# Performance work log

Hardware: AMD Instinct MI355X
Metric: run time of the kernel (lower is better)

Reference implementation:

```python
import jax, jax.numpy as jnp
import numpy as np

NUM_BINS = 30
MIN_BW = 0.001
MIN_BH = 0.001
MIN_D = 0.001
LI, UI = 0.0, 1.0   # input bounds
LO, UO = 0.0, 1.0   # output bounds
DERIV_OUT = (UO - LO) / (UI - LI)
EPS = 1e-6


def _cumparams(unnorm, lower, upper, min_size):
    # softmax -> min-size floor -> cumsum -> pad zero -> affine to [lower, upper]
    p = jax.nn.softmax(unnorm, axis=-1)
    p = min_size + (1.0 - min_size * NUM_BINS) * p
    cp = jnp.cumsum(p, axis=-1)
    cp = jnp.pad(cp, [(0, 0), (1, 0)])            # [V, nb+1], starts at 0
    cp = (upper - lower) * cp + lower
    return cp, cp[..., 1:] - cp[..., :-1]         # cum, bin sizes


def _spline_forward(inputs, uw, uh, ud):
    V = uw.shape[0]
    cw, widths = _cumparams(uw, LI, UI, MIN_BW)   # [V, nb+1], [V, nb]
    ch, heights = _cumparams(uh, LO, UO, MIN_BH)

    # boundary derivative constant: softplus(c) = 1 - MIN_D  =>  deriv = 1 at edges
    c = np.log(np.exp(1.0 - MIN_D) - 1.0).astype(np.float32)
    edge = jnp.full((V, 1), c, dtype=uw.dtype)
    derivs = MIN_D + jax.nn.softplus(jnp.concatenate([edge, ud, edge], axis=-1))  # [V, nb+1]

    delta = heights / widths                      # [V, nb]
    cb = cw.at[..., -1].add(EPS)                  # bin-search boundaries

    below = inputs < LI
    above = inputs > UI
    inside = ~(below | above)
    x = jnp.clip(inputs, LI, UI)                  # safe values for masked-out points

    # per-point bin search: [B, V, nb+1] comparison then sum
    bin_idx = jnp.sum(x[..., None] >= cb[None], axis=-1) - 1
    bin_idx = jnp.clip(bin_idx, 0, NUM_BINS - 1)  # [B, V] int

    v = jnp.arange(V)[None, :]
    icw = cw[v, bin_idx]
    ibw = widths[v, bin_idx]
    ich = ch[v, bin_idx]
    idl = delta[v, bin_idx]
    d0 = derivs[v, bin_idx]
    d1 = derivs[v, bin_idx + 1]
    ih = heights[v, bin_idx]

    theta = (x - icw) / ibw
    t1mt = theta * (1.0 - theta)
    den = idl + (d0 + d1 - 2.0 * idl) * t1mt
    out_in = ich + ih * (idl * theta * theta + d0 * t1mt) / den
    numd = (idl * idl) * (d1 * theta * theta + 2.0 * idl * t1mt + d0 * (1.0 - theta) ** 2)
    lad_in = jnp.log(numd) - 2.0 * jnp.log(den)

    out = jnp.where(below, LO + (inputs - LI) * DERIV_OUT,
          jnp.where(above, UO + (inputs - UI) * DERIV_OUT, out_in))
    lad = jnp.where(inside, lad_in, 0.0)
    return out, lad


def setup_inputs() -> dict:
    key = jax.random.key(0)
    k1, k2, k3, k4 = jax.random.split(key, 4)
    B, V = 16384, 512
    inputs = jax.random.uniform(k1, (B, V), dtype=jnp.float32)
    uw = 0.3 * jax.random.normal(k2, (V, NUM_BINS), dtype=jnp.float32)
    uh = 0.3 * jax.random.normal(k3, (V, NUM_BINS), dtype=jnp.float32)
    ud = 0.5405 + 0.1 * jax.random.normal(k4, (V, NUM_BINS - 1), dtype=jnp.float32)
    return {"inputs": inputs, "unnormalized_widths": uw,
            "unnormalized_heights": uh, "unnormalized_derivatives": ud}


def reference(inputs, unnormalized_widths, unnormalized_heights, unnormalized_derivatives):
    return _spline_forward(inputs, unnormalized_widths, unnormalized_heights,
                           unnormalized_derivatives)
```

## Files before the change

kernel.cpp:

```cpp
#include <hip/hip_runtime.h>
#include <math.h>

#define NB 30
#define PS 99
#define TPB 256

__device__ __forceinline__ float softplus_f(float x) {
    return fmaxf(x, 0.0f) + log1pf(__expf(-fabsf(x)));
}

__device__ __forceinline__ void stage_cum(const float* __restrict__ u, int v,
                                          float* __restrict__ dst) {
    float r[NB];
#pragma unroll
    for (int k = 0; k < NB; ++k) r[k] = u[v * NB + k];
    float m = r[0];
#pragma unroll
    for (int k = 1; k < NB; ++k) m = fmaxf(m, r[k]);
    float s = 0.f;
#pragma unroll
    for (int k = 0; k < NB; ++k) s += __expf(r[k] - m);
    const float fac = (1.0f - 0.001f * (float)NB) / s;
    float run = 0.f;
    dst[0] = 0.f;
#pragma unroll
    for (int k = 0; k < NB; ++k) {
        run += 0.001f + fac * __expf(r[k] - m);
        dst[3 * (k + 1)] = run;
    }
}

template <int VC, bool EXACT>
__global__ __launch_bounds__(TPB, 4) void rqs_fused_kernel(
        const float* __restrict__ x_in,
        const float* __restrict__ uw,
        const float* __restrict__ uh,
        const float* __restrict__ ud,
        float* __restrict__ out,
        float* __restrict__ lad,
        int B, int Vrt, int nct, int rowTiles) {
    const int V = VC ? VC : Vrt;

    __shared__ float pkS[64 * PS];

    const int tid = threadIdx.x;
    const int colTile = blockIdx.x % nct;
    const int rowBlk  = blockIdx.x / nct;
    const int colbase = colTile * 64;

    if (tid < 64) {
        const int v = colbase + tid;
        float* pcw = &pkS[tid * PS];
        stage_cum(uw, v, pcw);
        stage_cum(uh, v, pcw + 1);
        pcw[2] = 1.0f;
        pcw[3 * NB + 2] = 1.0f;
#pragma unroll
        for (int k = 1; k < NB; ++k)
            pcw[3 * k + 2] = 0.001f + softplus_f(ud[v * (NB - 1) + k - 1]);
        pcw[93] = 3.0e38f;
    }
    __syncthreads();

    const int c = tid & 63;
    const int w = tid >> 6;
    const int col = colbase + c;
    const float* __restrict__ pc = &pkS[c * PS];

    const float c12 = pc[12], c24 = pc[24], c36 = pc[36], c48 = pc[48];
    const float c60 = pc[60], c72 = pc[72], c84 = pc[84];

    const int passRows = 32;

    for (int base = rowBlk * passRows; base < B; base += rowTiles * passRows) {
        const int r0 = base + w * 8;

        float xv[8], xc[8];
        int jj[8];
#pragma unroll
        for (int u = 0; u < 8; ++u) {
            const int row = r0 + u;
            const bool ok = EXACT || (row < B);
            xv[u] = ok ? __builtin_nontemporal_load(&x_in[(size_t)row * V + col]) : 0.5f;
        }
#pragma unroll
        for (int u = 0; u < 8; ++u) xc[u] = fminf(fmaxf(xv[u], 0.0f), 1.0f);

#pragma unroll
        for (int u = 0; u < 8; ++u) {
            const float xq = xc[u];
            const bool b1 = (c48 <= xq);
            const float l2 = b1 ? c72 : c24;
            const bool b2 = (l2 <= xq);
            const float t0 = b2 ? c36 : c12;
            const float t1 = b2 ? c84 : c60;
            const float l3 = b1 ? t1 : t0;
            const bool b3 = (l3 <= xq);
            jj[u] = (b1 ? 48 : 0) + (b2 ? 24 : 0) + (b3 ? 12 : 0);
        }
#pragma unroll
        for (int u = 0; u < 8; ++u) jj[u] += (pc[jj[u] + 6] <= xc[u]) ? 6 : 0;
#pragma unroll
        for (int u = 0; u < 8; ++u) jj[u] += (pc[jj[u] + 3] <= xc[u]) ? 3 : 0;
#pragma unroll
        for (int u = 0; u < 8; ++u) jj[u] = min(jj[u], 3 * (NB - 1));

#pragma unroll
        for (int g = 0; g < 2; ++g) {
            float cwl[4], cwr[4], chl[4], chr[4], d0[4], d1[4];
#pragma unroll
            for (int q = 0; q < 4; ++q) {
                const float* p = pc + jj[g * 4 + q];
                cwl[q] = p[0]; cwr[q] = p[3];
                chl[q] = p[1]; chr[q] = p[4];
                d0[q]  = p[2]; d1[q]  = p[5];
            }
#pragma unroll
            for (int q = 0; q < 4; ++q) {
                const int u = g * 4 + q;
                const int row = r0 + u;
                const bool ok = EXACT || (row < B);
                const float wd = cwr[q] - cwl[q];
                const float h  = chr[q] - chl[q];
                const float winv = __builtin_amdgcn_rcpf(wd);
                const float delta = h * winv;
                const float theta = (xc[u] - cwl[q]) * winv;
                const float omt = 1.0f - theta;
                const float t1mt = theta * omt;
                const float th2 = theta * theta;
                const float den = delta + (d0[q] + d1[q] - 2.0f * delta) * t1mt;
                const float dinv = __builtin_amdgcn_rcpf(den);
                const float out_in = chl[q] + h * (delta * th2 + d0[q] * t1mt) * dinv;
                const float numd = delta * delta *
                    (d1[q] * th2 + 2.0f * delta * t1mt + d0[q] * omt * omt);
                const float lad_in = __logf(numd * dinv * dinv);

                const bool inside = (xv[u] >= 0.0f) && (xv[u] <= 1.0f);
                if (ok) {
                    const size_t idx = (size_t)row * V + col;
                    out[idx] = inside ? out_in : xv[u];
                    lad[idx] = inside ? lad_in : 0.0f;
                }
            }
        }
    }
}

extern "C" void kernel_launch(void* const* d_in, const int* in_sizes, int n_in,
                              void* d_out, int out_size, void* d_ws, size_t ws_size,
                              hipStream_t stream) {
    const float* x  = (const float*)d_in[0];
    const float* uw = (const float*)d_in[1];
    const float* uh = (const float*)d_in[2];
    const float* ud = (const float*)d_in[3];

    const int V = in_sizes[1] / NB;
    const int B = in_sizes[0] / V;

    float* out = (float*)d_out;
    float* lad = out + (size_t)B * V;

    if (V == 512 && (B % 32) == 0) {
        const int nct = 512 / 64;
        const int rowTiles = (B / 32 + 3) / 4 >= 128 ? 128 : (B / 32);
        rqs_fused_kernel<512, true><<<nct * rowTiles, TPB, 0, stream>>>(
            x, uw, uh, ud, out, lad, B, V, nct, rowTiles);
    } else {
        const int nct = V / 64;
        int rowTiles = (B + 31) / 32;
        if (rowTiles > 128) rowTiles = 128;
        rqs_fused_kernel<0, false><<<nct * rowTiles, TPB, 0, stream>>>(
            x, uw, uh, ud, out, lad, B, V, nct, rowTiles);
    }
}
```

Before: 35.34 us.

## Vectorize spline kernel with float4 row loads and software-prefetched row loop

Replaces the per-column scalar kernel with one where each thread handles four adjacent columns using 128-bit loads and stores. A loop over rows prefetches the next row's inputs, and the top three binary-search levels for each of the four columns stay in registers. The grid goes from 1024 to 1280 blocks, launch bounds rise to 5 waves, and a simpler generic fallback kernel is added. The aim is fewer, wider memory transactions and better latency hiding. In exchange, the four columns' parameters are read from strided LDS rows, which may cause bank conflicts, and register pressure from hb[4][7] rises.

```diff
diff --git a/kernel.cpp b/kernel.cpp
--- a/kernel.cpp
+++ b/kernel.cpp
@@ -4,6 +4,8 @@
 #define NB 30
 #define PS 99
 #define TPB 256
+
+typedef float f32x4 __attribute__((ext_vector_type(4)));
 
 __device__ __forceinline__ float softplus_f(float x) {
     return fmaxf(x, 0.0f) + log1pf(__expf(-fabsf(x)));
@@ -30,17 +32,136 @@
     }
 }
 
-template <int VC, bool EXACT>
-__global__ __launch_bounds__(TPB, 4) void rqs_fused_kernel(
-        const float* __restrict__ x_in,
-        const float* __restrict__ uw,
-        const float* __restrict__ uh,
-        const float* __restrict__ ud,
-        float* __restrict__ out,
-        float* __restrict__ lad,
-        int B, int Vrt, int nct, int rowTiles) {
-    const int V = VC ? VC : Vrt;
-
+__device__ __forceinline__ void col_params(const float* __restrict__ uw,
+                                           const float* __restrict__ uh,
+                                           const float* __restrict__ ud,
+                                           int v, float* __restrict__ pcw) {
+    stage_cum(uw, v, pcw);
+    stage_cum(uh, v, pcw + 1);
+    pcw[2] = 1.0f;
+    pcw[3 * NB + 2] = 1.0f;
+#pragma unroll
+    for (int k = 1; k < NB; ++k)
+        pcw[3 * k + 2] = 0.001f + softplus_f(ud[v * (NB - 1) + k - 1]);
+    pcw[93] = 3.0e38f;
+}
+
+__device__ __forceinline__ void spline_eval(float cwl, float chl, float d0,
+                                            float cwr, float chr, float d1,
+                                            float xq, float xraw,
+                                            float& o, float& ldv) {
+    const float wd = cwr - cwl;
+    const float h  = chr - chl;
+    const float winv = __builtin_amdgcn_rcpf(wd);
+    const float delta = h * winv;
+    const float theta = (xq - cwl) * winv;
+    const float omt = 1.0f - theta;
+    const float t1mt = theta * omt;
+    const float th2 = theta * theta;
+    const float den = delta + (d0 + d1 - 2.0f * delta) * t1mt;
+    const float dinv = __builtin_amdgcn_rcpf(den);
+    const float oi = chl + h * (delta * th2 + d0 * t1mt) * dinv;
+    const float numd = delta * delta * (d1 * th2 + 2.0f * delta * t1mt + d0 * omt * omt);
+    const float li = __logf(numd * dinv * dinv);
+    const bool inside = (xraw >= 0.0f) && (xraw <= 1.0f);
+    o   = inside ? oi : xraw;
+    ldv = inside ? li : 0.0f;
+}
+
+__global__ __launch_bounds__(TPB, 5) void rqs_vec_kernel(
+        const float* __restrict__ x_in, const float* __restrict__ uw,
+        const float* __restrict__ uh, const float* __restrict__ ud,
+        float* __restrict__ out, float* __restrict__ lad,
+        int B, int rowTiles) {
+    const int V = 512;
+    __shared__ float pkS[64 * PS];
+
+    const int tid = threadIdx.x;
+    const int colTile = blockIdx.x & 7;
+    const int rowBlk  = blockIdx.x >> 3;
+    const int colbase = colTile * 64;
+
+    if (tid < 64) col_params(uw, uh, ud, colbase + tid, &pkS[tid * PS]);
+    __syncthreads();
+
+    const int l = tid & 63;
+    const int w = tid >> 6;
+    const int g = (l & 15) * 4;
+    const int r = l >> 4;
+    const int col0 = colbase + g;
+    const float* __restrict__ pg = &pkS[g * PS];
+
+    float hb[4][7];
+#pragma unroll
+    for (int i = 0; i < 4; ++i)
+#pragma unroll
+        for (int t = 0; t < 7; ++t) hb[i][t] = pg[i * PS + 12 * (t + 1)];
+
+    const int rowStep = rowTiles * 16;
+    int row = rowBlk * 16 + w * 4 + r;
+    if (row >= B) return;
+    f32x4 xcur = *(const f32x4*)(x_in + (size_t)row * V + col0);
+
+    while (true) {
+        const int nrow = row + rowStep;
+        const bool has = (nrow < B);
+        f32x4 xnext;
+        if (has) xnext = *(const f32x4*)(x_in + (size_t)nrow * V + col0);
+
+        float xq[4];
+        int jj[4];
+#pragma unroll
+        for (int i = 0; i < 4; ++i) xq[i] = fminf(fmaxf(xcur[i], 0.0f), 1.0f);
+
+#pragma unroll
+        for (int i = 0; i < 4; ++i) {
+            const bool b1 = hb[i][3] <= xq[i];
+            const float l2 = b1 ? hb[i][5] : hb[i][1];
+            const bool b2 = l2 <= xq[i];
+            const float l3 = b1 ? (b2 ? hb[i][6] : hb[i][4])
+                               : (b2 ? hb[i][2] : hb[i][0]);
+            const bool b3 = l3 <= xq[i];
+            jj[i] = (b1 ? 48 : 0) + (b2 ? 24 : 0) + (b3 ? 12 : 0);
+        }
+#pragma unroll
+        for (int i = 0; i < 4; ++i) jj[i] += (pg[i * PS + jj[i] + 6] <= xq[i]) ? 6 : 0;
+#pragma unroll
+        for (int i = 0; i < 4; ++i) jj[i] += (pg[i * PS + jj[i] + 3] <= xq[i]) ? 3 : 0;
+#pragma unroll
+        for (int i = 0; i < 4; ++i) jj[i] = min(jj[i], 87) + i * PS;
+
+        float cwl[4], chl[4], d0a[4], cwr[4], chr[4], d1a[4];
+#pragma unroll
+        for (int i = 0; i < 4; ++i) {
+            const float* p = pg + jj[i];
+            cwl[i] = p[0]; chl[i] = p[1]; d0a[i] = p[2];
+            cwr[i] = p[3]; chr[i] = p[4]; d1a[i] = p[5];
+        }
+
+        f32x4 o, ldv;
+#pragma unroll
+        for (int i = 0; i < 4; ++i) {
+            float oi, li;
+            spline_eval(cwl[i], chl[i], d0a[i], cwr[i], chr[i], d1a[i],
+                        xq[i], xcur[i], oi, li);
+            o[i] = oi;
+            ldv[i] = li;
+        }
+
+        *(f32x4*)(out + (size_t)row * V + col0) = o;
+        *(f32x4*)(lad + (size_t)row * V + col0) = ldv;
+
+        if (!has) break;
+        row = nrow;
+        xcur = xnext;
+    }
+}
+
+__global__ __launch_bounds__(TPB, 4) void rqs_gen_kernel(
+        const float* __restrict__ x_in, const float* __restrict__ uw,
+        const float* __restrict__ uh, const float* __restrict__ ud,
+        float* __restrict__ out, float* __restrict__ lad,
+        int B, int V, int nct, int rowTiles) {
     __shared__ float pkS[64 * PS];
 
     const int tid = threadIdx.x;
@@ -48,101 +169,30 @@
     const int rowBlk  = blockIdx.x / nct;
     const int colbase = colTile * 64;
 
-    if (tid < 64) {
-        const int v = colbase + tid;
-        float* pcw = &pkS[tid * PS];
-        stage_cum(uw, v, pcw);
-        stage_cum(uh, v, pcw + 1);
-        pcw[2] = 1.0f;
-        pcw[3 * NB + 2] = 1.0f;
-#pragma unroll
-        for (int k = 1; k < NB; ++k)
-            pcw[3 * k + 2] = 0.001f + softplus_f(ud[v * (NB - 1) + k - 1]);
-        pcw[93] = 3.0e38f;
-    }
+    if (tid < 64 && colbase + tid < V)
+        col_params(uw, uh, ud, colbase + tid, &pkS[tid * PS]);
     __syncthreads();
 
     const int c = tid & 63;
     const int w = tid >> 6;
     const int col = colbase + c;
+    if (col >= V) return;
     const float* __restrict__ pc = &pkS[c * PS];
 
-    const float c12 = pc[12], c24 = pc[24], c36 = pc[36], c48 = pc[48];
-    const float c60 = pc[60], c72 = pc[72], c84 = pc[84];
-
-    const int passRows = 32;
-
-    for (int base = rowBlk * passRows; base < B; base += rowTiles * passRows) {
-        const int r0 = base + w * 8;
-
-        float xv[8], xc[8];
-        int jj[8];
-#pragma unroll
-        for (int u = 0; u < 8; ++u) {
-            const int row = r0 + u;
-            const bool ok = EXACT || (row < B);
-            xv[u] = ok ? __builtin_nontemporal_load(&x_in[(size_t)row * V + col]) : 0.5f;
-        }
-#pragma unroll
-        for (int u = 0; u < 8; ++u) xc[u] = fminf(fmaxf(xv[u], 0.0f), 1.0f);
-
-#pragma unroll
-        for (int u = 0; u < 8; ++u) {
-            const float xq = xc[u];
-            const bool b1 = (c48 <= xq);
-            const float l2 = b1 ? c72 : c24;
-            const bool b2 = (l2 <= xq);
-            const float t0 = b2 ? c36 : c12;
-            const float t1 = b2 ? c84 : c60;
-            const float l3 = b1 ? t1 : t0;
-            const bool b3 = (l3 <= xq);
-            jj[u] = (b1 ? 48 : 0) + (b2 ? 24 : 0) + (b3 ? 12 : 0);
-        }
-#pragma unroll
-        for (int u = 0; u < 8; ++u) jj[u] += (pc[jj[u] + 6] <= xc[u]) ? 6 : 0;
-#pragma unroll
-        for (int u = 0; u < 8; ++u) jj[u] += (pc[jj[u] + 3] <= xc[u]) ? 3 : 0;
-#pragma unroll
-        for (int u = 0; u < 8; ++u) jj[u] = min(jj[u], 3 * (NB - 1));
-
-#pragma unroll
-        for (int g = 0; g < 2; ++g) {
-            float cwl[4], cwr[4], chl[4], chr[4], d0[4], d1[4];
-#pragma unroll
-            for (int q = 0; q < 4; ++q) {
-                const float* p = pc + jj[g * 4 + q];
-                cwl[q] = p[0]; cwr[q] = p[3];
-                chl[q] = p[1]; chr[q] = p[4];
-                d0[q]  = p[2]; d1[q]  = p[5];
-            }
-#pragma unroll
-            for (int q = 0; q < 4; ++q) {
-                const int u = g * 4 + q;
-                const int row = r0 + u;
-                const bool ok = EXACT || (row < B);
-                const float wd = cwr[q] - cwl[q];
-                const float h  = chr[q] - chl[q];
-                const float winv = __builtin_amdgcn_rcpf(wd);
-                const float delta = h * winv;
-                const float theta = (xc[u] - cwl[q]) * winv;
-                const float omt = 1.0f - theta;
-                const float t1mt = theta * omt;
-                const float th2 = theta * theta;
-                const float den = delta + (d0[q] + d1[q] - 2.0f * delta) * t1mt;
-                const float dinv = __builtin_amdgcn_rcpf(den);
-                const float out_in = chl[q] + h * (delta * th2 + d0[q] * t1mt) * dinv;
-                const float numd = delta * delta *
-                    (d1[q] * th2 + 2.0f * delta * t1mt + d0[q] * omt * omt);
-                const float lad_in = __logf(numd * dinv * dinv);
-
-                const bool inside = (xv[u] >= 0.0f) && (xv[u] <= 1.0f);
-                if (ok) {
-                    const size_t idx = (size_t)row * V + col;
-                    out[idx] = inside ? out_in : xv[u];
-                    lad[idx] = inside ? lad_in : 0.0f;
-                }
-            }
-        }
+    for (int row = rowBlk * 4 + w; row < B; row += rowTiles * 4) {
+        const float xr = x_in[(size_t)row * V + col];
+        const float xq = fminf(fmaxf(xr, 0.0f), 1.0f);
+        int j = (pc[48] <= xq) ? 48 : 0;
+        j += (pc[j + 24] <= xq) ? 24 : 0;
+        j += (pc[j + 12] <= xq) ? 12 : 0;
+        j += (pc[j +  6] <= xq) ?  6 : 0;
+        j += (pc[j +  3] <= xq) ?  3 : 0;
+        j = min(j, 87);
+        const float* p = pc + j;
+        float o, ldv;
+        spline_eval(p[0], p[1], p[2], p[3], p[4], p[5], xq, xr, o, ldv);
+        out[(size_t)row * V + col] = o;
+        lad[(size_t)row * V + col] = ldv;
     }
 }
 
@@ -160,16 +210,15 @@
     float* out = (float*)d_out;
     float* lad = out + (size_t)B * V;
 
-    if (V == 512 && (B % 32) == 0) {
-        const int nct = 512 / 64;
-        const int rowTiles = (B / 32 + 3) / 4 >= 128 ? 128 : (B / 32);
-        rqs_fused_kernel<512, true><<<nct * rowTiles, TPB, 0, stream>>>(
+    if (V == 512 && (B % 16) == 0 && B >= 16) {
+        const int rowTiles = 160;
+        rqs_vec_kernel<<<8 * rowTiles, TPB, 0, stream>>>(
+            x, uw, uh, ud, out, lad, B, rowTiles);
+    } else {
+        const int nct = (V + 63) / 64;
+        int rowTiles = (B + 3) / 4;
+        if (rowTiles > 128) rowTiles = 128;
+        rqs_gen_kernel<<<nct * rowTiles, TPB, 0, stream>>>(
             x, uw, uh, ud, out, lad, B, V, nct, rowTiles);
-    } else {
-        const int nct = V / 64;
-        int rowTiles = (B + 31) / 32;
-        if (rowTiles > 128) rowTiles = 128;
-        rqs_fused_kernel<0, false><<<nct * rowTiles, TPB, 0, stream>>>(
-            x, uw, uh, ud, out, lad, B, V, nct, rowTiles);
-    }
-}
+    }
+}
```

Measured after the change: 41.41 us. +17.2%, slower.
